# Kernel tuning notes

Hardware: AMD Instinct MI355X
Metric: run time of the kernel (lower is better)

The kernel has to match this reference:

```python
import jax, jax.numpy as jnp
import numpy as np

N = 50000
E = 800000
IN_DIM, HID, OUT = 128, 256, 256


def setup_inputs() -> dict:
    key = jax.random.key(0)
    ks = jax.random.split(key, 6)
    x = jax.random.normal(ks[0], (N, IN_DIM), dtype=jnp.float32)
    edge_index = jax.random.randint(ks[1], (2, E), 0, N, dtype=jnp.int64)
    W1 = jax.random.normal(ks[2], (IN_DIM, HID), dtype=jnp.float32) / np.sqrt(IN_DIM)
    b1 = jnp.zeros((HID,), dtype=jnp.float32)
    W2 = jax.random.normal(ks[3], (HID, OUT), dtype=jnp.float32) / np.sqrt(HID)
    b2 = jnp.zeros((OUT,), dtype=jnp.float32)
    return {"x": x, "edge_index": edge_index, "W1": W1, "b1": b1, "W2": W2, "b2": b2}


def _gcn_conv(x, edge_index, W, b):
    """PyG GCNConv: add self-loops, symmetric deg^-1/2 norm, linear, scatter-add, bias."""
    n = x.shape[0]
    loops = jnp.arange(n, dtype=edge_index.dtype)
    src = jnp.concatenate([edge_index[0], loops])  # [E+N]
    dst = jnp.concatenate([edge_index[1], loops])  # [E+N]
    deg = jax.ops.segment_sum(jnp.ones(src.shape[0], dtype=x.dtype), dst, num_segments=n)
    dinv = jnp.where(deg > 0, jax.lax.rsqrt(deg), jnp.zeros_like(deg))
    norm = dinv[src] * dinv[dst]  # [E+N]
    h = x @ W  # [N, out] small GEMM before gather (PyG order)
    msg = h[src] * norm[:, None]  # [E+N, out] -- dominant memory traffic
    out = jax.ops.segment_sum(msg, dst, num_segments=n)
    return out + b


def reference(x, edge_index, W1, b1, W2, b2):
    h = jax.nn.relu(_gcn_conv(x, edge_index, W1, b1))
    # dropout is identity in eval mode
    out = _gcn_conv(h, edge_index, W2, b2)
    # F.normalize(p=2, dim=-1, eps=1e-12)
    nrm = jnp.maximum(jnp.linalg.norm(out, axis=-1, keepdims=True), 1e-12)
    return out / nrm
```

## Files before the change

kernel.cpp:

```cpp
#include <hip/hip_runtime.h>
#include <hip/hip_bf16.h>


#define NNODE 50000
#define FDIM 256
#define SCAN_CHUNK 2048
#define CAST_BLOCKS 3125
#define WCONV_BLOCKS 48

typedef __attribute__((ext_vector_type(8))) short short8;
typedef __attribute__((ext_vector_type(4))) float f32x4;

__device__ __forceinline__ float bflo(unsigned int u) {
    union { unsigned int i; float f; } c;
    c.i = u << 16;
    return c.f;
}
__device__ __forceinline__ float bfhi(unsigned int u) {
    union { unsigned int i; float f; } c;
    c.i = u & 0xFFFF0000u;
    return c.f;
}
__device__ __forceinline__ unsigned short f2bf(float f) {
    __hip_bfloat16 h = __float2bfloat16(f);
    return *reinterpret_cast<unsigned short*>(&h);
}
__device__ __forceinline__ unsigned int pk(float lo, float hi) {
    return (unsigned int)f2bf(lo) | ((unsigned int)f2bf(hi) << 16);
}

__global__ __launch_bounds__(256) void prep_kernel(
    const float* __restrict__ x, unsigned int* __restrict__ xb,
    const float* __restrict__ W1, unsigned short* __restrict__ Wf1,
    const float* __restrict__ W2, unsigned short* __restrict__ Wf2,
    const int* __restrict__ ei, int* __restrict__ counts, int E) {
    int b = blockIdx.x, t = threadIdx.x;
    if (b < CAST_BLOCKS) {
        int i = b * 256 + t;
        const float4* xf = reinterpret_cast<const float4*>(x);
        float4 p = xf[2 * i], q = xf[2 * i + 1];
        uint4 o;
        o.x = pk(p.x, p.y); o.y = pk(p.z, p.w);
        o.z = pk(q.x, q.y); o.w = pk(q.z, q.w);
        reinterpret_cast<uint4*>(xb)[i] = o;
    } else if (b < CAST_BLOCKS + WCONV_BLOCKS) {
        int idx = (b - CAST_BLOCKS) * 256 + t;
        const float* W;
        unsigned short* Wf;
        if (idx < 16 * 256) { W = W1; Wf = Wf1; }
        else { idx -= 16 * 256; W = W2; Wf = Wf2; }
        int g = idx >> 8, c = idx & 255;
        ushort4 lo = make_ushort4(f2bf(W[(8 * g + 0) * 256 + c]), f2bf(W[(8 * g + 1) * 256 + c]),
                                  f2bf(W[(8 * g + 2) * 256 + c]), f2bf(W[(8 * g + 3) * 256 + c]));
        ushort4 hi = make_ushort4(f2bf(W[(8 * g + 4) * 256 + c]), f2bf(W[(8 * g + 5) * 256 + c]),
                                  f2bf(W[(8 * g + 6) * 256 + c]), f2bf(W[(8 * g + 7) * 256 + c]));
        *reinterpret_cast<ushort4*>(&Wf[(size_t)idx * 8]) = lo;
        *reinterpret_cast<ushort4*>(&Wf[(size_t)idx * 8 + 4]) = hi;
    } else {
        int e = (b - CAST_BLOCKS - WCONV_BLOCKS) * 256 + t;
        if (e < E) atomicAdd(&counts[ei[E + e]], 1);
    }
}

__global__ __launch_bounds__(256) void scan_part1(const int* __restrict__ counts,
                                                  int* __restrict__ bsum, int n) {
    __shared__ int ws[4];
    int b = blockIdx.x, t = threadIdx.x;
    int base = b * SCAN_CHUNK + t * 8;
    int s = 0;
#pragma unroll
    for (int j = 0; j < 8; ++j) {
        int i = base + j;
        if (i < n) s += counts[i];
    }
#pragma unroll
    for (int off = 32; off >= 1; off >>= 1) s += __shfl_xor(s, off, 64);
    if ((t & 63) == 0) ws[t >> 6] = s;
    __syncthreads();
    if (t == 0) bsum[b] = ws[0] + ws[1] + ws[2] + ws[3];
}

__global__ void scan_part2(const int* __restrict__ bsum, int* __restrict__ boff,
                           int* __restrict__ row_ptr, int nb, int n) {
    int l = threadIdx.x;
    int v = (l < nb) ? bsum[l] : 0;
    int incl = v;
#pragma unroll
    for (int off = 1; off < 64; off <<= 1) {
        int u = __shfl_up(incl, off, 64);
        if (l >= off) incl += u;
    }
    if (l < nb) boff[l] = incl - v;
    if (l == nb - 1) row_ptr[n] = incl;
}

__global__ __launch_bounds__(256) void scan_part3(const int* __restrict__ counts,
                                                  const int* __restrict__ boff,
                                                  int* __restrict__ row_ptr,
                                                  int* __restrict__ cursor,
                                                  float* __restrict__ dinv, int n) {
    __shared__ int ws[4];
    int b = blockIdx.x, t = threadIdx.x, lane = t & 63, wid = t >> 6;
    int base = b * SCAN_CHUNK + t * 8;
    int v[8];
    int s = 0;
#pragma unroll
    for (int j = 0; j < 8; ++j) {
        int i = base + j;
        v[j] = (i < n) ? counts[i] : 0;
        s += v[j];
    }
    int incl = s;
#pragma unroll
    for (int off = 1; off < 64; off <<= 1) {
        int u = __shfl_up(incl, off, 64);
        if (lane >= off) incl += u;
    }
    if (lane == 63) ws[wid] = incl;
    __syncthreads();
    int woff = 0;
    for (int u = 0; u < wid; ++u) woff += ws[u];
    int ex = boff[b] + woff + incl - s;
#pragma unroll
    for (int j = 0; j < 8; ++j) {
        int i = base + j;
        if (i < n) {
            row_ptr[i] = ex;
            cursor[i] = ex;
            dinv[i] = rsqrtf((float)(v[j] + 1));
        }
        ex += v[j];
    }
}

__global__ void fill_kernel(const int* __restrict__ ei, const float* __restrict__ dinv,
                            int* __restrict__ cursor, int2* __restrict__ edata, int E) {
    int e = blockIdx.x * blockDim.x + threadIdx.x;
    if (e < E) {
        int s = ei[e];
        int d = ei[E + e];
        int pos = atomicAdd(&cursor[d], 1);
        float nm = dinv[s] * dinv[d];
        edata[pos] = make_int2(s, __float_as_int(nm));
    }
}

__global__ __launch_bounds__(256) void agg1_kernel(const unsigned int* __restrict__ xb,
                                                   const int* __restrict__ rowp,
                                                   const int2* __restrict__ edata,
                                                   const float* __restrict__ dinv,
                                                   unsigned int* __restrict__ A1, int n) {
    int node = (blockIdx.x * blockDim.x + threadIdx.x) >> 6;
    int lane = threadIdx.x & 63;
    if (node >= n) return;
    float di = dinv[node];
    float d2 = di * di;
    unsigned int sv = xb[(size_t)node * 64 + lane];
    float a0 = bflo(sv) * d2, a1 = bfhi(sv) * d2;
    int beg = rowp[node], end = rowp[node + 1];
#pragma unroll 4
    for (int e = beg; e < end; ++e) {
        int2 ed = edata[e];
        float nm = __int_as_float(ed.y);
        unsigned int v = xb[(size_t)ed.x * 64 + lane];
        a0 = fmaf(bflo(v), nm, a0);
        a1 = fmaf(bfhi(v), nm, a1);
    }
    A1[(size_t)node * 64 + lane] = pk(a0, a1);
}

__global__ __launch_bounds__(256) void agg2_kernel(const uint2* __restrict__ hb,
                                                   const int* __restrict__ rowp,
                                                   const int2* __restrict__ edata,
                                                   const float* __restrict__ dinv,
                                                   uint2* __restrict__ A2, int n) {
    int node = (blockIdx.x * blockDim.x + threadIdx.x) >> 6;
    int lane = threadIdx.x & 63;
    if (node >= n) return;
    float di = dinv[node];
    float d2 = di * di;
    uint2 sv = hb[(size_t)node * 64 + lane];
    float a0 = bflo(sv.x) * d2, a1 = bfhi(sv.x) * d2;
    float a2 = bflo(sv.y) * d2, a3 = bfhi(sv.y) * d2;
    int beg = rowp[node], end = rowp[node + 1];
#pragma unroll 4
    for (int e = beg; e < end; ++e) {
        int2 ed = edata[e];
        float nm = __int_as_float(ed.y);
        uint2 v = hb[(size_t)ed.x * 64 + lane];
        a0 = fmaf(bflo(v.x), nm, a0);
        a1 = fmaf(bfhi(v.x), nm, a1);
        a2 = fmaf(bflo(v.y), nm, a2);
        a3 = fmaf(bfhi(v.y), nm, a3);
    }
    uint2 o;
    o.x = pk(a0, a1);
    o.y = pk(a2, a3);
    A2[(size_t)node * 64 + lane] = o;
}

template <int K, int EPI>
__global__ __launch_bounds__(256) void gemm_fused(const unsigned short* __restrict__ A,
                                                  const unsigned short* __restrict__ Wf,
                                                  const float* __restrict__ bias,
                                                  void* __restrict__ outp, int n) {
    __shared__ unsigned short As[64 * K];
    __shared__ __align__(16) float ssred[64][4];
    int t = threadIdx.x;
    int row0 = blockIdx.x * 64;

#pragma unroll
    for (int i = 0; i < (64 * K) / (8 * 256); ++i) {
        int o = 8 * (t + 256 * i);
        int row = o / K, k = o % K;
        int srow = row0 + row;
        uint4 v = make_uint4(0u, 0u, 0u, 0u);
        if (srow < n) v = *reinterpret_cast<const uint4*>(&A[(size_t)srow * K + k]);
        int gx = (k >> 3) ^ (row & 7);
        *reinterpret_cast<uint4*>(&As[row * K + gx * 8]) = v;
    }
    __syncthreads();

    int lane = t & 63, wv = t >> 6;
    int l15 = lane & 15, lhi = lane >> 4;
    f32x4 zero = {0.f, 0.f, 0.f, 0.f};
    f32x4 acc[4][4];
#pragma unroll
    for (int rf = 0; rf < 4; ++rf)
#pragma unroll
        for (int cf = 0; cf < 4; ++cf) acc[rf][cf] = zero;

#pragma unroll
    for (int s = 0; s < K / 32; ++s) {
        int g = 4 * s + lhi;
        short8 a[4], b[4];
#pragma unroll
        for (int rf = 0; rf < 4; ++rf) {
            int row = 16 * rf + l15;
            a[rf] = *reinterpret_cast<const short8*>(&As[row * K + (g ^ (row & 7)) * 8]);
        }
#pragma unroll
        for (int cf = 0; cf < 4; ++cf) {
            int c = 64 * wv + 16 * cf + l15;
            b[cf] = *reinterpret_cast<const short8*>(&Wf[((size_t)g * 256 + c) * 8]);
        }
#pragma unroll
        for (int rf = 0; rf < 4; ++rf)
#pragma unroll
            for (int cf = 0; cf < 4; ++cf)
                acc[rf][cf] = __builtin_amdgcn_mfma_f32_16x16x32_bf16(a[rf], b[cf], acc[rf][cf], 0, 0, 0);
    }

    if constexpr (EPI == 0) {
        unsigned short* H = (unsigned short*)outp;
#pragma unroll
        for (int cf = 0; cf < 4; ++cf) {
            int col = 64 * wv + 16 * cf + l15;
            float bc = bias[col];
#pragma unroll
            for (int rf = 0; rf < 4; ++rf) {
#pragma unroll
                for (int j = 0; j < 4; ++j) {
                    int row = row0 + 16 * rf + 4 * lhi + j;
                    if (row < n) H[(size_t)row * 256 + col] = f2bf(fmaxf(acc[rf][cf][j] + bc, 0.f));
                }
            }
        }
    } else {
        float* O = (float*)outp;
        float ss[4][4];
#pragma unroll
        for (int rf = 0; rf < 4; ++rf)
#pragma unroll
            for (int j = 0; j < 4; ++j) ss[rf][j] = 0.f;
#pragma unroll
        for (int cf = 0; cf < 4; ++cf) {
            int col = 64 * wv + 16 * cf + l15;
            float bc = bias[col];
#pragma unroll
            for (int rf = 0; rf < 4; ++rf)
#pragma unroll
                for (int j = 0; j < 4; ++j) {
                    float v = acc[rf][cf][j] + bc;
                    acc[rf][cf][j] = v;
                    ss[rf][j] = fmaf(v, v, ss[rf][j]);
                }
        }
#pragma unroll
        for (int rf = 0; rf < 4; ++rf)
#pragma unroll
            for (int j = 0; j < 4; ++j) {
#pragma unroll
                for (int off = 1; off <= 8; off <<= 1)
                    ss[rf][j] += __shfl_xor(ss[rf][j], off, 64);
            }
        if (l15 == 0) {
#pragma unroll
            for (int rf = 0; rf < 4; ++rf)
#pragma unroll
                for (int j = 0; j < 4; ++j) ssred[16 * rf + 4 * lhi + j][wv] = ss[rf][j];
        }
        __syncthreads();
        float rinv[4][4];
#pragma unroll
        for (int rf = 0; rf < 4; ++rf)
#pragma unroll
            for (int j = 0; j < 4; ++j) {
                float4 s4 = *reinterpret_cast<const float4*>(ssred[16 * rf + 4 * lhi + j]);
                float tot = s4.x + s4.y + s4.z + s4.w;
                rinv[rf][j] = 1.f / fmaxf(sqrtf(tot), 1e-12f);
            }
#pragma unroll
        for (int cf = 0; cf < 4; ++cf) {
            int col = 64 * wv + 16 * cf + l15;
#pragma unroll
            for (int rf = 0; rf < 4; ++rf)
#pragma unroll
                for (int j = 0; j < 4; ++j) {
                    int row = row0 + 16 * rf + 4 * lhi + j;
                    if (row < n) O[(size_t)row * 256 + col] = acc[rf][cf][j] * rinv[rf][j];
                }
        }
    }
}

extern "C" void kernel_launch(void* const* d_in, const int* in_sizes, int n_in,
                              void* d_out, int out_size, void* d_ws, size_t ws_size,
                              hipStream_t stream) {
    const float* x  = (const float*)d_in[0];
    const int*   ei = (const int*)d_in[1];
    const float* W1 = (const float*)d_in[2];
    const float* b1 = (const float*)d_in[3];
    const float* W2 = (const float*)d_in[4];
    const float* b2 = (const float*)d_in[5];
    float* out = (float*)d_out;

    const int N = NNODE;
    const int E = in_sizes[1] / 2;
    const int NB = (N + SCAN_CHUNK - 1) / SCAN_CHUNK;

    char* ws = (char*)d_ws;
    size_t off = 0;
    auto alloc = [&](size_t bytes) -> void* {
        void* p = ws + off;
        off = (off + bytes + 255) & ~(size_t)255;
        return p;
    };
    unsigned int*   xb  = (unsigned int*)alloc((size_t)N * 128 * 2);
    unsigned int*   A1  = (unsigned int*)alloc((size_t)N * 128 * 2);
    unsigned short* Bbf = (unsigned short*)alloc((size_t)N * FDIM * 2);
    uint2*          A2  = (uint2*)alloc((size_t)N * FDIM * 2);
    unsigned short* Wf1 = (unsigned short*)alloc((size_t)16 * 256 * 8 * 2);
    unsigned short* Wf2 = (unsigned short*)alloc((size_t)32 * 256 * 8 * 2);
    int*   counts = (int*)alloc((size_t)N * 4);
    int*   rowp   = (int*)alloc((size_t)(N + 1) * 4);
    int*   cursor = (int*)alloc((size_t)N * 4);
    float* dinv   = (float*)alloc((size_t)N * 4);
    int2*  edata  = (int2*)alloc((size_t)E * 8);
    int*   bsum   = (int*)alloc((size_t)NB * 4);
    int*   boff   = (int*)alloc((size_t)NB * 4);

    hipMemsetAsync(counts, 0, (size_t)N * 4, stream);
    int count_blocks = (E + 255) / 256;
    prep_kernel<<<CAST_BLOCKS + WCONV_BLOCKS + count_blocks, 256, 0, stream>>>(
        x, xb, W1, Wf1, W2, Wf2, ei, counts, E);
    scan_part1<<<NB, 256, 0, stream>>>(counts, bsum, N);
    scan_part2<<<1, 64, 0, stream>>>(bsum, boff, rowp, NB, N);
    scan_part3<<<NB, 256, 0, stream>>>(counts, boff, rowp, cursor, dinv, N);
    fill_kernel<<<(E + 255) / 256, 256, 0, stream>>>(ei, dinv, cursor, edata, E);

    agg1_kernel<<<(N * 64 + 255) / 256, 256, 0, stream>>>(xb, rowp, edata, dinv, A1, N);
    gemm_fused<128, 0><<<(N + 63) / 64, 256, 0, stream>>>(
        (const unsigned short*)A1, Wf1, b1, Bbf, N);
    agg2_kernel<<<(N * 64 + 255) / 256, 256, 0, stream>>>(
        (const uint2*)Bbf, rowp, edata, dinv, A2, N);
    gemm_fused<256, 1><<<(N + 63) / 64, 256, 0, stream>>>(
        (const unsigned short*)A2, Wf2, b2, out, N);
}
```

Baseline: 258.4 us.

## Fold block scan into scan_part3, vectorize bf16 epilogue stores with permuted W2

Removes the single-block scan_part2 launch by having every scan_part3 block recompute the block-offset prefix over bsum itself. The layer-1 GEMM epilogue now packs four bf16 columns into one 8-byte store, which changes the column order of the hidden features. W2's rows are permuted during the weight conversion to match that order. The aggregation loops are unrolled further, and the final output uses nontemporal stores. This trims launch overhead and uncoalesced 2-byte stores, at the cost of redundant scan work per block and more reliance on the layout permutation being exactly right.

```diff
diff --git a/kernel.cpp b/kernel.cpp
--- a/kernel.cpp
+++ b/kernel.cpp
@@ -47,15 +47,21 @@
         int idx = (b - CAST_BLOCKS) * 256 + t;
         const float* W;
         unsigned short* Wf;
-        if (idx < 16 * 256) { W = W1; Wf = Wf1; }
-        else { idx -= 16 * 256; W = W2; Wf = Wf2; }
+        bool perm;
+        if (idx < 16 * 256) { W = W1; Wf = Wf1; perm = false; }
+        else { idx -= 16 * 256; W = W2; Wf = Wf2; perm = true; }
         int g = idx >> 8, c = idx & 255;
-        ushort4 lo = make_ushort4(f2bf(W[(8 * g + 0) * 256 + c]), f2bf(W[(8 * g + 1) * 256 + c]),
-                                  f2bf(W[(8 * g + 2) * 256 + c]), f2bf(W[(8 * g + 3) * 256 + c]));
-        ushort4 hi = make_ushort4(f2bf(W[(8 * g + 4) * 256 + c]), f2bf(W[(8 * g + 5) * 256 + c]),
-                                  f2bf(W[(8 * g + 6) * 256 + c]), f2bf(W[(8 * g + 7) * 256 + c]));
-        *reinterpret_cast<ushort4*>(&Wf[(size_t)idx * 8]) = lo;
-        *reinterpret_cast<ushort4*>(&Wf[(size_t)idx * 8 + 4]) = hi;
+        unsigned short vals[8];
+#pragma unroll
+        for (int j = 0; j < 8; ++j) {
+            int k = 8 * g + j;
+            int f = perm ? ((k & ~63) | ((k & 3) << 4) | ((k >> 2) & 15)) : k;
+            vals[j] = f2bf(W[(size_t)f * 256 + c]);
+        }
+        *reinterpret_cast<ushort4*>(&Wf[(size_t)idx * 8]) =
+            make_ushort4(vals[0], vals[1], vals[2], vals[3]);
+        *reinterpret_cast<ushort4*>(&Wf[(size_t)idx * 8 + 4]) =
+            make_ushort4(vals[4], vals[5], vals[6], vals[7]);
     } else {
         int e = (b - CAST_BLOCKS - WCONV_BLOCKS) * 256 + t;
         if (e < E) atomicAdd(&counts[ei[E + e]], 1);
@@ -80,27 +86,29 @@
     if (t == 0) bsum[b] = ws[0] + ws[1] + ws[2] + ws[3];
 }
 
-__global__ void scan_part2(const int* __restrict__ bsum, int* __restrict__ boff,
-                           int* __restrict__ row_ptr, int nb, int n) {
-    int l = threadIdx.x;
-    int v = (l < nb) ? bsum[l] : 0;
-    int incl = v;
-#pragma unroll
-    for (int off = 1; off < 64; off <<= 1) {
-        int u = __shfl_up(incl, off, 64);
-        if (l >= off) incl += u;
-    }
-    if (l < nb) boff[l] = incl - v;
-    if (l == nb - 1) row_ptr[n] = incl;
-}
-
 __global__ __launch_bounds__(256) void scan_part3(const int* __restrict__ counts,
-                                                  const int* __restrict__ boff,
+                                                  const int* __restrict__ bsum,
                                                   int* __restrict__ row_ptr,
                                                   int* __restrict__ cursor,
-                                                  float* __restrict__ dinv, int n) {
+                                                  float* __restrict__ dinv,
+                                                  int n, int nb) {
     __shared__ int ws[4];
+    __shared__ int s_boff, s_total;
     int b = blockIdx.x, t = threadIdx.x, lane = t & 63, wid = t >> 6;
+    if (t < 64) {
+        int v = (t < nb) ? bsum[t] : 0;
+        int incl = v;
+#pragma unroll
+        for (int off = 1; off < 64; off <<= 1) {
+            int u = __shfl_up(incl, off, 64);
+            if (t >= off) incl += u;
+        }
+        if (t == b) s_boff = incl - v;
+        if (t == nb - 1) s_total = incl;
+    }
+    __syncthreads();
+    if (b == 0 && t == 0) row_ptr[n] = s_total;
+
     int base = b * SCAN_CHUNK + t * 8;
     int v[8];
     int s = 0;
@@ -120,7 +128,7 @@
     __syncthreads();
     int woff = 0;
     for (int u = 0; u < wid; ++u) woff += ws[u];
-    int ex = boff[b] + woff + incl - s;
+    int ex = s_boff + woff + incl - s;
 #pragma unroll
     for (int j = 0; j < 8; ++j) {
         int i = base + j;
@@ -158,7 +166,7 @@
     unsigned int sv = xb[(size_t)node * 64 + lane];
     float a0 = bflo(sv) * d2, a1 = bfhi(sv) * d2;
     int beg = rowp[node], end = rowp[node + 1];
-#pragma unroll 4
+#pragma unroll 8
     for (int e = beg; e < end; ++e) {
         int2 ed = edata[e];
         float nm = __int_as_float(ed.y);
@@ -183,7 +191,7 @@
     float a0 = bflo(sv.x) * d2, a1 = bfhi(sv.x) * d2;
     float a2 = bflo(sv.y) * d2, a3 = bfhi(sv.y) * d2;
     int beg = rowp[node], end = rowp[node + 1];
-#pragma unroll 4
+#pragma unroll 8
     for (int e = beg; e < end; ++e) {
         int2 ed = edata[e];
         float nm = __int_as_float(ed.y);
@@ -253,16 +261,23 @@
 
     if constexpr (EPI == 0) {
         unsigned short* H = (unsigned short*)outp;
-#pragma unroll
-        for (int cf = 0; cf < 4; ++cf) {
-            int col = 64 * wv + 16 * cf + l15;
-            float bc = bias[col];
-#pragma unroll
-            for (int rf = 0; rf < 4; ++rf) {
-#pragma unroll
-                for (int j = 0; j < 4; ++j) {
-                    int row = row0 + 16 * rf + 4 * lhi + j;
-                    if (row < n) H[(size_t)row * 256 + col] = f2bf(fmaxf(acc[rf][cf][j] + bc, 0.f));
+        float bv[4];
+#pragma unroll
+        for (int cf = 0; cf < 4; ++cf) bv[cf] = bias[64 * wv + 16 * cf + l15];
+#pragma unroll
+        for (int rf = 0; rf < 4; ++rf) {
+#pragma unroll
+            for (int j = 0; j < 4; ++j) {
+                int row = row0 + 16 * rf + 4 * lhi + j;
+                if (row < n) {
+                    float c0 = fmaxf(acc[rf][0][j] + bv[0], 0.f);
+                    float c1 = fmaxf(acc[rf][1][j] + bv[1], 0.f);
+                    float c2 = fmaxf(acc[rf][2][j] + bv[2], 0.f);
+                    float c3 = fmaxf(acc[rf][3][j] + bv[3], 0.f);
+                    uint2 o;
+                    o.x = pk(c0, c1);
+                    o.y = pk(c2, c3);
+                    *reinterpret_cast<uint2*>(&H[(size_t)row * 256 + 64 * wv + 4 * l15]) = o;
                 }
             }
         }
@@ -318,7 +333,9 @@
 #pragma unroll
                 for (int j = 0; j < 4; ++j) {
                     int row = row0 + 16 * rf + 4 * lhi + j;
-                    if (row < n) O[(size_t)row * 256 + col] = acc[rf][cf][j] * rinv[rf][j];
+                    if (row < n)
+                        __builtin_nontemporal_store(acc[rf][cf][j] * rinv[rf][j],
+                                                    &O[(size_t)row * 256 + col]);
                 }
         }
     }
@@ -358,15 +375,13 @@
     float* dinv   = (float*)alloc((size_t)N * 4);
     int2*  edata  = (int2*)alloc((size_t)E * 8);
     int*   bsum   = (int*)alloc((size_t)NB * 4);
-    int*   boff   = (int*)alloc((size_t)NB * 4);
 
     hipMemsetAsync(counts, 0, (size_t)N * 4, stream);
     int count_blocks = (E + 255) / 256;
     prep_kernel<<<CAST_BLOCKS + WCONV_BLOCKS + count_blocks, 256, 0, stream>>>(
         x, xb, W1, Wf1, W2, Wf2, ei, counts, E);
     scan_part1<<<NB, 256, 0, stream>>>(counts, bsum, N);
-    scan_part2<<<1, 64, 0, stream>>>(bsum, boff, rowp, NB, N);
-    scan_part3<<<NB, 256, 0, stream>>>(counts, boff, rowp, cursor, dinv, N);
+    scan_part3<<<NB, 256, 0, stream>>>(counts, bsum, rowp, cursor, dinv, N, NB);
     fill_kernel<<<(E + 255) / 256, 256, 0, stream>>>(ei, dinv, cursor, edata, E);
 
     agg1_kernel<<<(N * 64 + 255) / 256, 256, 0, stream>>>(xb, rowp, edata, dinv, A1, N);
```

After: 246.7 us. 1.05x faster.
